# Optimization experiments

Hardware: AMD Instinct MI355X
Metric: run time of the kernel (lower is better)

The kernel has to match this reference:

```python
import jax, jax.numpy as jnp
import numpy as np

HEAD_DIM = 64
NUM_Q_HEADS = 32
NUM_KV_HEADS = 8
ROPE_FREQ = 10000.0
EPS = 1e-6


def _rms_norm(x, gamma):
    # normalize over last dim (head_dim)
    var = jnp.mean(jnp.square(x), axis=-1, keepdims=True)
    return x * jax.lax.rsqrt(var + EPS) * gamma


def _rope_cos_sin(seq_len, dtype=jnp.float32):
    inv_freq = 1.0 / (ROPE_FREQ ** (jnp.arange(0, HEAD_DIM, 2, dtype=jnp.float32) / HEAD_DIM))
    pos = jnp.arange(seq_len, dtype=jnp.float32)
    freqs = pos[:, None] * inv_freq[None, :]          # [S, hd/2]
    emb = jnp.concatenate([freqs, freqs], axis=-1)    # [S, hd]
    return jnp.cos(emb).astype(dtype), jnp.sin(emb).astype(dtype)


def _rotate_half(x):
    x1, x2 = jnp.split(x, 2, axis=-1)
    return jnp.concatenate([-x2, x1], axis=-1)


def _apply_rope(x, cos, sin):
    # x: [B, H, S, hd]; cos/sin: [S, hd]
    return x * cos[None, None, :, :] + _rotate_half(x) * sin[None, None, :, :]


def setup_inputs() -> dict:
    key = jax.random.key(0)
    ks = jax.random.split(key, 5)
    B, S, D = 2, 2048, 2048
    qkv_out = (NUM_Q_HEADS + 2 * NUM_KV_HEADS) * HEAD_DIM  # 3072
    x = jax.random.normal(ks[0], (B, S, D), dtype=jnp.float32)
    w_qkv = jax.random.normal(ks[1], (qkv_out, D), dtype=jnp.float32) * (D ** -0.5)
    w_out = jax.random.normal(ks[2], (D, NUM_Q_HEADS * HEAD_DIM), dtype=jnp.float32) * ((NUM_Q_HEADS * HEAD_DIM) ** -0.5)
    q_gamma = jnp.ones((HEAD_DIM,), dtype=jnp.float32)
    k_gamma = jnp.ones((HEAD_DIM,), dtype=jnp.float32)
    return {"x": x, "w_qkv": w_qkv, "w_out": w_out, "q_gamma": q_gamma, "k_gamma": k_gamma}


def reference(x, w_qkv, w_out, q_gamma, k_gamma):
    B, S, D = x.shape
    groups = NUM_Q_HEADS // NUM_KV_HEADS
    # fused QKV projection (no bias)
    qkv = jnp.einsum("bsd,od->bso", x, w_qkv)
    qkv = qkv.reshape(B, S, NUM_Q_HEADS + 2 * NUM_KV_HEADS, HEAD_DIM)
    qkv = jnp.transpose(qkv, (0, 2, 1, 3))  # [B, heads, S, hd]
    q = qkv[:, :NUM_Q_HEADS]
    k = qkv[:, NUM_Q_HEADS:NUM_Q_HEADS + NUM_KV_HEADS]
    v = qkv[:, NUM_Q_HEADS + NUM_KV_HEADS:]
    # QK RMSNorm over head_dim
    q = _rms_norm(q, q_gamma)
    k = _rms_norm(k, k_gamma)
    # RoPE
    cos, sin = _rope_cos_sin(S, dtype=x.dtype)
    q = _apply_rope(q, cos, sin)
    k = _apply_rope(k, cos, sin)
    # GQA: repeat-interleave kv heads
    k = jnp.repeat(k, groups, axis=1)
    v = jnp.repeat(v, groups, axis=1)
    # causal SDPA
    scale = HEAD_DIM ** -0.5
    scores = jnp.einsum("bhqd,bhkd->bhqk", q, k) * scale
    causal = jnp.tril(jnp.ones((S, S), dtype=bool))
    scores = jnp.where(causal[None, None], scores, jnp.finfo(scores.dtype).min)
    attn = jax.nn.softmax(scores, axis=-1)
    ctx = jnp.einsum("bhqk,bhkd->bhqd", attn, v)
    ctx = jnp.transpose(ctx, (0, 2, 1, 3)).reshape(B, S, NUM_Q_HEADS * HEAD_DIM)
    out = jnp.einsum("bsf,df->bsd", ctx, w_out)
    return out
```

## Files before the change

kernel.cpp:

```cpp
#include <hip/hip_runtime.h>

typedef _Float16 f16;
typedef __fp16 fp16x2 __attribute__((ext_vector_type(2)));
typedef _Float16 f16x8 __attribute__((ext_vector_type(8)));
typedef float f32x4 __attribute__((ext_vector_type(4)));
typedef float f32x16 __attribute__((ext_vector_type(16)));

#define AS1 __attribute__((address_space(1)))
#define AS3 __attribute__((address_space(3)))

#define SCALE_L2E 0.18033688011112042f


__device__ __forceinline__ void gload16(const void* g, void* l) {
    __builtin_amdgcn_global_load_lds(
        (const AS1 unsigned*)(unsigned long long)g,
        (AS3 unsigned*)(unsigned)(unsigned long long)l,
        16, 0, 0);
}

__device__ __forceinline__ unsigned pk2(float a, float b) {
    union { fp16x2 v; unsigned u; } c;
    c.v = __builtin_amdgcn_cvt_pkrtz(a, b);
    return c.u;
}

#define BAR() do { asm volatile("" ::: "memory"); __builtin_amdgcn_s_barrier(); asm volatile("" ::: "memory"); } while (0)


__global__ __launch_bounds__(256) void k_cast_all(const float* __restrict__ x,
                                                  const float* __restrict__ wq,
                                                  const float* __restrict__ wo,
                                                  f16* __restrict__ Xh,
                                                  f16* __restrict__ Wqh,
                                                  f16* __restrict__ Woh,
                                                  float* __restrict__ cosT,
                                                  float* __restrict__ sinT) {
    if (blockIdx.x >= 18432) {
        int idx = (blockIdx.x - 18432) * 256 + threadIdx.x;
        int s = idx >> 5, i = idx & 31;
        float ang = (float)s * exp2f(-(float)i * 0.4152410118609190f);
        cosT[idx] = cosf(ang);
        sinT[idx] = sinf(ang);
        return;
    }
    int i = (blockIdx.x * 256 + threadIdx.x) * 4;
    const float* src; f16* dst;
    if (i < 8388608)        { src = x  + i;            dst = Xh  + i; }
    else if (i < 14680064)  { src = wq + (i - 8388608); dst = Wqh + (i - 8388608); }
    else                    { src = wo + (i - 14680064); dst = Woh + (i - 14680064); }
    float4 v = *(const float4*)src;
    union { f16 h[4]; ushort4 u; } c;
    c.h[0] = (f16)v.x; c.h[1] = (f16)v.y; c.h[2] = (f16)v.z; c.h[3] = (f16)v.w;
    *(ushort4*)dst = c.u;
}


template <typename OutT, int BH>
__global__ __launch_bounds__(512, 2) void k_gemm256(const f16* __restrict__ A,
                                                    const f16* __restrict__ Bt,
                                                    OutT* __restrict__ C,
                                                    int M, int N, int K) {
    constexpr int BUFSZ = 32768 + BH * 16384;
    constexpr int NN = 2 * BH;
    __shared__ __align__(16) char sm[2 * BUFSZ];
    const int tid = threadIdx.x;
    const int lane = tid & 63, wid = tid >> 6;
    const int wm = wid >> 2, wn = wid & 3;
    const int lr = lane & 15, g4 = lane >> 4;

    const int gx = gridDim.x;
    const int nwg = gx * gridDim.y;
    int lin = blockIdx.y * gx + blockIdx.x;
    lin = (lin & 7) * (nwg >> 3) + (lin >> 3);
    const int bx = lin % gx, by = lin / gx;
    const int m0 = by * 256, n0 = bx * (128 * BH);
    const int NT = K >> 6;

    const int srow = tid >> 3;
    const int scol = ((tid & 7) ^ (srow & 7)) * 8;
    const f16* gA = A  + (size_t)(m0 + srow) * K + scol;
    const f16* gB = Bt + (size_t)(n0 + srow) * K + scol;

    auto STGA = [&](int t, int h) {
        char* d = sm + (t & 1) * BUFSZ + h * 16384 + tid * 16;
        gload16(gA + (size_t)(h * 128) * K + t * 64,      d);
        gload16(gA + (size_t)(h * 128 + 64) * K + t * 64, d + 8192);
    };
    auto STGB = [&](int t, int h) {
        char* d = sm + (t & 1) * BUFSZ + 32768 + h * 16384 + tid * 16;
        gload16(gB + (size_t)(h * 128) * K + t * 64,      d);
        gload16(gB + (size_t)(h * 128 + 64) * K + t * 64, d + 8192);
    };

    f32x4 acc[8][NN] = {};
    f16x8 bfr[NN];

    STGA(0, 0); STGA(0, 1); STGB(0, 0); if (BH == 2) STGB(0, 1);
    STGA(1, 0); STGA(1, 1); STGB(1, 0); if (BH == 2) STGB(1, 1);
    if constexpr (BH == 2) asm volatile("s_waitcnt vmcnt(8)" ::: "memory");
    else                   asm volatile("s_waitcnt vmcnt(6)" ::: "memory");
    BAR();

    for (int t = 0; t < NT; ++t) {
        const int buf = t & 1;
        const char* bA = sm + buf * BUFSZ + wm * 16384;
        const char* bB = sm + buf * BUFSZ + 32768 + (BH == 2 ? (wn >> 1) * 16384 : 0);
        const bool sA = (t >= 1) && (t + 1 < NT);
        const bool sB = (t + 2 < NT);
#pragma unroll
        for (int p = 0; p < 4; ++p) {
            const int kk = p >> 1, mh = p & 1;
            f16x8 afr[4];
            if (mh == 0) {
#pragma unroll
                for (int n = 0; n < NN; n++) {
                    const int r = (BH == 2 ? (wn & 1) * 64 : wn * 32) + n * 16 + lr;
                    bfr[n] = *(const f16x8*)(bB + ((r * 128 + kk * 64 + g4 * 16) ^ ((r & 7) << 4)));
                }
            }
#pragma unroll
            for (int i = 0; i < 4; i++) {
                const int r = (mh * 4 + i) * 16 + lr;
                afr[i] = *(const f16x8*)(bA + ((r * 128 + kk * 64 + g4 * 16) ^ ((r & 7) << 4)));
            }
            if (p == 0 && sA) STGA(t + 1, 0);
            if (p == 1 && sA) STGA(t + 1, 1);
            if (p == 3 && sB) { STGB(t + 2, 0); if (BH == 2) STGB(t + 2, 1); }
            BAR();
            asm volatile("s_waitcnt lgkmcnt(0)" ::: "memory");
            __builtin_amdgcn_s_setprio(1);
#pragma unroll
            for (int i = 0; i < 4; i++)
#pragma unroll
                for (int n = 0; n < NN; n++)
                    acc[mh * 4 + i][n] = __builtin_amdgcn_mfma_f32_16x16x32_f16(afr[i], bfr[n], acc[mh * 4 + i][n], 0, 0, 0);
            __builtin_amdgcn_s_setprio(0);
            if (p == 3 && t + 1 < NT) {
                if (t + 2 < NT) {
                    if constexpr (BH == 2) asm volatile("s_waitcnt vmcnt(4)" ::: "memory");
                    else                   asm volatile("s_waitcnt vmcnt(2)" ::: "memory");
                } else {
                    asm volatile("s_waitcnt vmcnt(0)" ::: "memory");
                }
            }
            BAR();
        }
    }

#pragma unroll
    for (int m = 0; m < 8; m++)
#pragma unroll
        for (int n = 0; n < NN; n++) {
            size_t base = (size_t)(m0 + wm * 128 + m * 16 + g4 * 4) * N + (n0 + wn * (32 * BH) + n * 16 + lr);
#pragma unroll
            for (int j = 0; j < 4; j++)
                C[base + (size_t)j * N] = (OutT)acc[m][n][j];
        }
}


__global__ __launch_bounds__(256) void k_qkv_post(const f16* __restrict__ qkv,
                                                  const float* __restrict__ qg,
                                                  const float* __restrict__ kg,
                                                  const float* __restrict__ cosT,
                                                  const float* __restrict__ sinT,
                                                  f16* __restrict__ Qf,
                                                  f16* __restrict__ Kf,
                                                  f16* __restrict__ Vf) {
    __shared__ f16 tl[4][8][72];
    const int tid = threadIdx.x, lane = tid & 63, wv = tid >> 6;
    const int gw = blockIdx.x * 4 + wv;
    const int b = gw / 12288;
    const int r0 = gw - b * 12288;
    const int head = r0 >> 8;
    const int sblk = r0 & 255;
    const int s0 = sblk * 8;
    const int s_loc = lane >> 3, ch = lane & 7;
    const int s = s0 + s_loc;

    f16x8 v = *(const f16x8*)&qkv[((size_t)b * 2048 + s) * 3072 + head * 64 + ch * 8];

    if (head < 40) {
        float vf[8];
#pragma unroll
        for (int j = 0; j < 8; j++) vf[j] = (float)v[j];
        float ss = 0.f;
#pragma unroll
        for (int j = 0; j < 8; j++) ss += vf[j] * vf[j];
        ss += __shfl_xor(ss, 1); ss += __shfl_xor(ss, 2); ss += __shfl_xor(ss, 4);
        float rinv = rsqrtf(ss * (1.0f / 64.0f) + 1e-6f);
        const float* gam = (head < 32 ? qg : kg) + ch * 8;
        float4 g0 = *(const float4*)gam, g1 = *(const float4*)(gam + 4);
        float gv[8] = {g0.x, g0.y, g0.z, g0.w, g1.x, g1.y, g1.z, g1.w};
        float xn[8], ot[8];
#pragma unroll
        for (int j = 0; j < 8; j++) xn[j] = vf[j] * rinv * gv[j];
#pragma unroll
        for (int j = 0; j < 8; j++) ot[j] = __shfl_xor(xn[j], 4);
        const int i0 = (ch & 3) * 8;
        float4 c0  = *(const float4*)&cosT[(s << 5) + i0];
        float4 c1  = *(const float4*)&cosT[(s << 5) + i0 + 4];
        float4 sn0 = *(const float4*)&sinT[(s << 5) + i0];
        float4 sn1 = *(const float4*)&sinT[(s << 5) + i0 + 4];
        float cs[8] = {c0.x, c0.y, c0.z, c0.w, c1.x, c1.y, c1.z, c1.w};
        float sn[8] = {sn0.x, sn0.y, sn0.z, sn0.w, sn1.x, sn1.y, sn1.z, sn1.w};
        float sgn = (ch < 4) ? -1.0f : 1.0f;
        float ov[8];
#pragma unroll
        for (int j = 0; j < 8; j++) ov[j] = xn[j] * cs[j] + sgn * ot[j] * sn[j];
        if (head < 32) {
#pragma unroll
            for (int j = 0; j < 8; j++) ov[j] *= SCALE_L2E;
        }
        uint4 o;
        o.x = pk2(ov[0], ov[1]); o.y = pk2(ov[2], ov[3]);
        o.z = pk2(ov[4], ov[5]); o.w = pk2(ov[6], ov[7]);
        const int t = s >> 5;
        const int lane2 = (s & 31) + ((ch & 1) << 5);
        const int c = ch >> 1;
        f16* dst = (head < 32)
            ? Qf + (((size_t)(b * 32 + head) * 256 + t * 4 + c) * 512 + lane2 * 8)
            : Kf + (((size_t)(b * 8 + head - 32) * 256 + t * 4 + c) * 512 + lane2 * 8);
        *(uint4*)dst = o;
    } else {
        const int kh = head - 40;
        *(f16x8*)&tl[wv][s_loc][ch * 8] = v;
        asm volatile("s_waitcnt lgkmcnt(0)" ::: "memory");
        f16x8 cv;
#pragma unroll
        for (int rr = 0; rr < 8; rr++) cv[rr] = tl[wv][rr][lane];
        const int d = lane, dh = d >> 5;
        const int t = s0 >> 5, c = (s0 >> 4) & 1, hv = (s0 >> 3) & 1;
        const int g = dh * 2 + c;
        f16* dst = Vf + (((size_t)(b * 8 + kh) * 256 + t * 4 + g) * 512
                         + ((d & 31) + (hv << 5)) * 8);
        *(f16x8*)dst = cv;
    }
}


struct AttnPart { f32x16 o0, o1; float l; };

__device__ __forceinline__ AttnPart attn_part(int qb, int par, int lane, int lq, int hi,
        const f16* __restrict__ Qfp, const f16* __restrict__ Kfp,
        const f16* __restrict__ Vfp) {
    f16x8 qf[4];
#pragma unroll
    for (int c = 0; c < 4; c++)
        qf[c] = *(const f16x8*)&Qfp[((size_t)qb * 4 + c) * 512 + lane * 8];

    AttnPart P;
    P.o0 = (f32x16){}; P.o1 = (f32x16){};
    float lrun = 0.0f;

    f16x8 kf[4], va[2], vb[2];
    if (par <= qb) {
#pragma unroll
        for (int c = 0; c < 4; c++)
            kf[c] = *(const f16x8*)&Kfp[((size_t)par * 4 + c) * 512 + lane * 8];
#pragma unroll
        for (int c = 0; c < 2; c++) {
            va[c] = *(const f16x8*)&Vfp[((size_t)par * 4 + c)     * 512 + lane * 8];
            vb[c] = *(const f16x8*)&Vfp[((size_t)par * 4 + 2 + c) * 512 + lane * 8];
        }
    }

    for (int kt = par; kt <= qb; kt += 2) {
        f32x16 st = {};
#pragma unroll
        for (int c = 0; c < 4; c++)
            st = __builtin_amdgcn_mfma_f32_32x32x16_f16(kf[c], qf[c], st, 0, 0, 0);

        if (kt + 2 <= qb) {
#pragma unroll
            for (int c = 0; c < 4; c++)
                kf[c] = *(const f16x8*)&Kfp[((size_t)(kt + 2) * 4 + c) * 512 + lane * 8];
        }

        if (kt == qb) {
#pragma unroll
            for (int r = 0; r < 16; r++) {
                int kvl = (r & 3) + ((r >> 2) << 3) + (hi << 2);
                if (kvl > lq) st[r] = -1e30f;
            }
        }

        unsigned X[8];
        float ps0 = 0.0f, ps1 = 0.0f;
#pragma unroll
        for (int j = 0; j < 8; j++) {
            float p0 = __builtin_amdgcn_exp2f(st[2 * j]);
            float p1 = __builtin_amdgcn_exp2f(st[2 * j + 1]);
            ps0 += p0; ps1 += p1;
            X[j] = pk2(p0, p1);
        }
        lrun += ps0 + ps1;

#pragma unroll
        for (int c = 0; c < 2; c++) {
            unsigned a0 = X[4 * c], a1 = X[4 * c + 1], a2 = X[4 * c + 2], a3 = X[4 * c + 3];
            asm volatile("v_permlane32_swap_b32 %0, %1" : "+v"(a0), "+v"(a2));
            asm volatile("v_permlane32_swap_b32 %0, %1" : "+v"(a1), "+v"(a3));
            union { unsigned u[4]; f16x8 v; } pb;
            pb.u[0] = a0; pb.u[1] = a1; pb.u[2] = a2; pb.u[3] = a3;
            P.o0 = __builtin_amdgcn_mfma_f32_32x32x16_f16(va[c], pb.v, P.o0, 0, 0, 0);
            P.o1 = __builtin_amdgcn_mfma_f32_32x32x16_f16(vb[c], pb.v, P.o1, 0, 0, 0);
        }
        if (kt + 2 <= qb) {
#pragma unroll
            for (int c = 0; c < 2; c++) {
                va[c] = *(const f16x8*)&Vfp[((size_t)(kt + 2) * 4 + c)     * 512 + lane * 8];
                vb[c] = *(const f16x8*)&Vfp[((size_t)(kt + 2) * 4 + 2 + c) * 512 + lane * 8];
            }
        }
    }

    P.l = lrun + __shfl_xor(lrun, 32);
    return P;
}

__global__ __launch_bounds__(128) void k_attn(const f16* __restrict__ Qf,
                                              const f16* __restrict__ Kf,
                                              const f16* __restrict__ Vf,
                                              f16* __restrict__ ctx) {
    __shared__ float ldsO[32][65];
    __shared__ float ldsL[32];
    const int tid = threadIdx.x;
    const int par = tid >> 6, lane = tid & 63;
    const int lq = lane & 31, hi = lane >> 5;
    const int bh = blockIdx.y, b = bh >> 5, h = bh & 31, kh = h >> 2;
    const int pj = blockIdx.x;

    const f16* Qfp = Qf + (size_t)(b * 32 + h) * 131072;
    const f16* Kfp = Kf + (size_t)(b * 8 + kh) * 131072;
    const f16* Vfp = Vf + (size_t)(b * 8 + kh) * 131072;
    f16*       ctxbase = ctx + (size_t)b * 2048 * 2048 + h * 64;

    const int qbs[2] = {pj, 63 - pj};
#pragma unroll
    for (int s = 0; s < 2; s++) {
        const int qb = qbs[s];
        AttnPart P = attn_part(qb, par, lane, lq, hi, Qfp, Kfp, Vfp);

        if (par == 1) {
            if (hi == 0) ldsL[lq] = P.l;
#pragma unroll
            for (int r = 0; r < 16; r++) {
                int d = (r & 3) + ((r >> 2) << 3) + (hi << 2);
                ldsO[lq][d]      = P.o0[r];
                ldsO[lq][d + 32] = P.o1[r];
            }
        }
        __syncthreads();
        if (par == 0) {
            float inv = 1.0f / (P.l + ldsL[lq]);
            unsigned* row = (unsigned*)(ctxbase + (size_t)(qb * 32 + lq) * 2048);
#pragma unroll
            for (int g = 0; g < 4; g++) {
                int d = 8 * g + 4 * hi;
                float c0 = (P.o0[4 * g]     + ldsO[lq][d])     * inv;
                float c1 = (P.o0[4 * g + 1] + ldsO[lq][d + 1]) * inv;
                float c2 = (P.o0[4 * g + 2] + ldsO[lq][d + 2]) * inv;
                float c3 = (P.o0[4 * g + 3] + ldsO[lq][d + 3]) * inv;
                uint2 a; a.x = pk2(c0, c1); a.y = pk2(c2, c3);
                *(uint2*)(row + 2 * hi + 4 * g) = a;
                float e0 = (P.o1[4 * g]     + ldsO[lq][d + 32]) * inv;
                float e1 = (P.o1[4 * g + 1] + ldsO[lq][d + 33]) * inv;
                float e2 = (P.o1[4 * g + 2] + ldsO[lq][d + 34]) * inv;
                float e3 = (P.o1[4 * g + 3] + ldsO[lq][d + 35]) * inv;
                uint2 e; e.x = pk2(e0, e1); e.y = pk2(e2, e3);
                *(uint2*)(row + 16 + 2 * hi + 4 * g) = e;
            }
        }
        __syncthreads();
    }
}


extern "C" void kernel_launch(void* const* d_in, const int* in_sizes, int n_in,
                              void* d_out, int out_size, void* d_ws, size_t ws_size,
                              hipStream_t stream) {
    const float* x     = (const float*)d_in[0];
    const float* w_qkv = (const float*)d_in[1];
    const float* w_out = (const float*)d_in[2];
    const float* qg    = (const float*)d_in[3];
    const float* kg    = (const float*)d_in[4];
    float* out = (float*)d_out;
    char* ws = (char*)d_ws;

    float* cosT = (float*)(ws);
    float* sinT = (float*)(ws + 262144);
    f16* Xh     = (f16*)(ws + 524288);
    f16* Wqkvh  = (f16*)(ws + 17301504);
    f16* Wouth  = (f16*)(ws + 29884416);
    f16* QKVh   = (f16*)(ws + 38273024);
    f16* Qfb    = (f16*)(ws + 63438848);
    f16* Kfb    = (f16*)(ws + 80216064);
    f16* Vfb    = (f16*)(ws + 84410368);
    f16* Ctxh   = (f16*)(ws + 88604672);

    k_cast_all<<<18688, 256, 0, stream>>>(x, w_qkv, w_out, Xh, Wqkvh, Wouth, cosT, sinT);

    k_gemm256<f16, 2><<<dim3(12, 16), 512, 0, stream>>>(Xh, Wqkvh, QKVh, 4096, 3072, 2048);

    k_qkv_post<<<6144, 256, 0, stream>>>(QKVh, qg, kg, cosT, sinT, Qfb, Kfb, Vfb);

    k_attn<<<dim3(32, 64), 128, 0, stream>>>(Qfb, Kfb, Vfb, Ctxh);

    k_gemm256<float, 1><<<dim3(16, 16), 512, 0, stream>>>(Ctxh, Wouth, out, 4096, 2048, 2048);
}
```

Measured before the change: 198.2 us.

## Generalize GEMM N-tile width and double-buffer K/V tiles in attention loop

The GEMM template now parameterizes its N tile in 64-column units. The QKV projection uses 192-wide tiles on a 16x16 grid, giving 256 workgroups instead of 192 so the CUs are filled more evenly. The output GEMM keeps its 128-wide tile through the new NU=2 path, with adjusted vmcnt waits. The attention inner loop is unrolled by two with separate register sets for K and V, so the score MFMA for the second tile overlaps the exp and PV of the first, at the cost of more registers.

```diff
diff --git a/kernel.cpp b/kernel.cpp
--- a/kernel.cpp
+++ b/kernel.cpp
@@ -56,13 +56,12 @@
 }
 
 
-template <typename OutT, int BH>
+template <typename OutT, int NU>
 __global__ __launch_bounds__(512, 2) void k_gemm256(const f16* __restrict__ A,
                                                     const f16* __restrict__ Bt,
                                                     OutT* __restrict__ C,
                                                     int M, int N, int K) {
-    constexpr int BUFSZ = 32768 + BH * 16384;
-    constexpr int NN = 2 * BH;
+    constexpr int BUFSZ = 32768 + NU * 8192;
     __shared__ __align__(16) char sm[2 * BUFSZ];
     const int tid = threadIdx.x;
     const int lane = tid & 63, wid = tid >> 6;
@@ -74,7 +73,7 @@
     int lin = blockIdx.y * gx + blockIdx.x;
     lin = (lin & 7) * (nwg >> 3) + (lin >> 3);
     const int bx = lin % gx, by = lin / gx;
-    const int m0 = by * 256, n0 = bx * (128 * BH);
+    const int m0 = by * 256, n0 = bx * (64 * NU);
     const int NT = K >> 6;
 
     const int srow = tid >> 3;
@@ -87,25 +86,26 @@
         gload16(gA + (size_t)(h * 128) * K + t * 64,      d);
         gload16(gA + (size_t)(h * 128 + 64) * K + t * 64, d + 8192);
     };
-    auto STGB = [&](int t, int h) {
-        char* d = sm + (t & 1) * BUFSZ + 32768 + h * 16384 + tid * 16;
-        gload16(gB + (size_t)(h * 128) * K + t * 64,      d);
-        gload16(gB + (size_t)(h * 128 + 64) * K + t * 64, d + 8192);
+    auto STGB = [&](int t) {
+#pragma unroll
+        for (int u = 0; u < NU; u++)
+            gload16(gB + (size_t)(u * 64) * K + t * 64,
+                    sm + (t & 1) * BUFSZ + 32768 + u * 8192 + tid * 16);
     };
 
-    f32x4 acc[8][NN] = {};
-    f16x8 bfr[NN];
-
-    STGA(0, 0); STGA(0, 1); STGB(0, 0); if (BH == 2) STGB(0, 1);
-    STGA(1, 0); STGA(1, 1); STGB(1, 0); if (BH == 2) STGB(1, 1);
-    if constexpr (BH == 2) asm volatile("s_waitcnt vmcnt(8)" ::: "memory");
-    else                   asm volatile("s_waitcnt vmcnt(6)" ::: "memory");
+    f32x4 acc[8][NU] = {};
+    f16x8 bfr[NU];
+
+    STGA(0, 0); STGA(0, 1); STGB(0);
+    STGA(1, 0); STGA(1, 1); STGB(1);
+    if constexpr (NU == 2) asm volatile("s_waitcnt vmcnt(6)" ::: "memory");
+    else                   asm volatile("s_waitcnt vmcnt(7)" ::: "memory");
     BAR();
 
     for (int t = 0; t < NT; ++t) {
         const int buf = t & 1;
         const char* bA = sm + buf * BUFSZ + wm * 16384;
-        const char* bB = sm + buf * BUFSZ + 32768 + (BH == 2 ? (wn >> 1) * 16384 : 0);
+        const char* bB = sm + buf * BUFSZ + 32768;
         const bool sA = (t >= 1) && (t + 1 < NT);
         const bool sB = (t + 2 < NT);
 #pragma unroll
@@ -114,8 +114,8 @@
             f16x8 afr[4];
             if (mh == 0) {
 #pragma unroll
-                for (int n = 0; n < NN; n++) {
-                    const int r = (BH == 2 ? (wn & 1) * 64 : wn * 32) + n * 16 + lr;
+                for (int n = 0; n < NU; n++) {
+                    const int r = wn * (16 * NU) + n * 16 + lr;
                     bfr[n] = *(const f16x8*)(bB + ((r * 128 + kk * 64 + g4 * 16) ^ ((r & 7) << 4)));
                 }
             }
@@ -126,20 +126,20 @@
             }
             if (p == 0 && sA) STGA(t + 1, 0);
             if (p == 1 && sA) STGA(t + 1, 1);
-            if (p == 3 && sB) { STGB(t + 2, 0); if (BH == 2) STGB(t + 2, 1); }
+            if (p == 3 && sB) STGB(t + 2);
             BAR();
             asm volatile("s_waitcnt lgkmcnt(0)" ::: "memory");
             __builtin_amdgcn_s_setprio(1);
 #pragma unroll
             for (int i = 0; i < 4; i++)
 #pragma unroll
-                for (int n = 0; n < NN; n++)
+                for (int n = 0; n < NU; n++)
                     acc[mh * 4 + i][n] = __builtin_amdgcn_mfma_f32_16x16x32_f16(afr[i], bfr[n], acc[mh * 4 + i][n], 0, 0, 0);
             __builtin_amdgcn_s_setprio(0);
             if (p == 3 && t + 1 < NT) {
                 if (t + 2 < NT) {
-                    if constexpr (BH == 2) asm volatile("s_waitcnt vmcnt(4)" ::: "memory");
-                    else                   asm volatile("s_waitcnt vmcnt(2)" ::: "memory");
+                    if constexpr (NU == 2) asm volatile("s_waitcnt vmcnt(2)" ::: "memory");
+                    else                   asm volatile("s_waitcnt vmcnt(3)" ::: "memory");
                 } else {
                     asm volatile("s_waitcnt vmcnt(0)" ::: "memory");
                 }
@@ -151,8 +151,8 @@
 #pragma unroll
     for (int m = 0; m < 8; m++)
 #pragma unroll
-        for (int n = 0; n < NN; n++) {
-            size_t base = (size_t)(m0 + wm * 128 + m * 16 + g4 * 4) * N + (n0 + wn * (32 * BH) + n * 16 + lr);
+        for (int n = 0; n < NU; n++) {
+            size_t base = (size_t)(m0 + wm * 128 + m * 16 + g4 * 4) * N + (n0 + wn * (16 * NU) + n * 16 + lr);
 #pragma unroll
             for (int j = 0; j < 4; j++)
                 C[base + (size_t)j * N] = (OutT)acc[m][n][j];
@@ -242,6 +242,40 @@
 
 struct AttnPart { f32x16 o0, o1; float l; };
 
+__device__ __forceinline__ void do_exp(const f32x16& st, unsigned* X, float& lrun) {
+    float ps0 = 0.0f, ps1 = 0.0f;
+#pragma unroll
+    for (int j = 0; j < 8; j++) {
+        float p0 = __builtin_amdgcn_exp2f(st[2 * j]);
+        float p1 = __builtin_amdgcn_exp2f(st[2 * j + 1]);
+        ps0 += p0; ps1 += p1;
+        X[j] = pk2(p0, p1);
+    }
+    lrun += ps0 + ps1;
+}
+
+__device__ __forceinline__ void do_pv(const f16x8* va, const f16x8* vb,
+                                      const unsigned* X, f32x16& o0, f32x16& o1) {
+#pragma unroll
+    for (int c = 0; c < 2; c++) {
+        unsigned a0 = X[4 * c], a1 = X[4 * c + 1], a2 = X[4 * c + 2], a3 = X[4 * c + 3];
+        asm volatile("v_permlane32_swap_b32 %0, %1" : "+v"(a0), "+v"(a2));
+        asm volatile("v_permlane32_swap_b32 %0, %1" : "+v"(a1), "+v"(a3));
+        union { unsigned u[4]; f16x8 v; } pb;
+        pb.u[0] = a0; pb.u[1] = a1; pb.u[2] = a2; pb.u[3] = a3;
+        o0 = __builtin_amdgcn_mfma_f32_32x32x16_f16(va[c], pb.v, o0, 0, 0, 0);
+        o1 = __builtin_amdgcn_mfma_f32_32x32x16_f16(vb[c], pb.v, o1, 0, 0, 0);
+    }
+}
+
+__device__ __forceinline__ void do_mask(f32x16& st, int lq, int hi) {
+#pragma unroll
+    for (int r = 0; r < 16; r++) {
+        int kvl = (r & 3) + ((r >> 2) << 3) + (hi << 2);
+        if (kvl > lq) st[r] = -1e30f;
+    }
+}
+
 __device__ __forceinline__ AttnPart attn_part(int qb, int par, int lane, int lq, int hi,
         const f16* __restrict__ Qfp, const f16* __restrict__ Kfp,
         const f16* __restrict__ Vfp) {
@@ -254,66 +288,62 @@
     P.o0 = (f32x16){}; P.o1 = (f32x16){};
     float lrun = 0.0f;
 
-    f16x8 kf[4], va[2], vb[2];
-    if (par <= qb) {
+    f16x8 kfa[4], kfb[4], vaa[2], vba[2], vab[2], vbb[2];
+
+    auto LOADK = [&](f16x8* kf, int t) {
 #pragma unroll
         for (int c = 0; c < 4; c++)
-            kf[c] = *(const f16x8*)&Kfp[((size_t)par * 4 + c) * 512 + lane * 8];
+            kf[c] = *(const f16x8*)&Kfp[((size_t)t * 4 + c) * 512 + lane * 8];
+    };
+    auto LOADV = [&](f16x8* va, f16x8* vb, int t) {
 #pragma unroll
         for (int c = 0; c < 2; c++) {
-            va[c] = *(const f16x8*)&Vfp[((size_t)par * 4 + c)     * 512 + lane * 8];
-            vb[c] = *(const f16x8*)&Vfp[((size_t)par * 4 + 2 + c) * 512 + lane * 8];
-        }
-    }
-
-    for (int kt = par; kt <= qb; kt += 2) {
+            va[c] = *(const f16x8*)&Vfp[((size_t)t * 4 + c)     * 512 + lane * 8];
+            vb[c] = *(const f16x8*)&Vfp[((size_t)t * 4 + 2 + c) * 512 + lane * 8];
+        }
+    };
+
+    int kt = par;
+    if (kt <= qb)     { LOADK(kfa, kt);     LOADV(vaa, vba, kt); }
+    if (kt + 2 <= qb) { LOADK(kfb, kt + 2); LOADV(vab, vbb, kt + 2); }
+
+    while (kt + 2 <= qb) {
+        const int nx = kt + 4;
+        f32x16 sta = {};
+#pragma unroll
+        for (int c = 0; c < 4; c++)
+            sta = __builtin_amdgcn_mfma_f32_32x32x16_f16(kfa[c], qf[c], sta, 0, 0, 0);
+        unsigned Xa[8];
+        do_exp(sta, Xa, lrun);
+
+        f32x16 stb = {};
+#pragma unroll
+        for (int c = 0; c < 4; c++)
+            stb = __builtin_amdgcn_mfma_f32_32x32x16_f16(kfb[c], qf[c], stb, 0, 0, 0);
+        if (nx <= qb) LOADK(kfa, nx);
+
+        do_pv(vaa, vba, Xa, P.o0, P.o1);
+        if (nx <= qb) LOADV(vaa, vba, nx);
+
+        if (kt + 2 == qb) do_mask(stb, lq, hi);
+        unsigned Xb[8];
+        do_exp(stb, Xb, lrun);
+        if (nx + 2 <= qb) LOADK(kfb, nx + 2);
+
+        do_pv(vab, vbb, Xb, P.o0, P.o1);
+        if (nx + 2 <= qb) LOADV(vab, vbb, nx + 2);
+
+        kt = nx;
+    }
+    if (kt <= qb) {
         f32x16 st = {};
 #pragma unroll
         for (int c = 0; c < 4; c++)
-            st = __builtin_amdgcn_mfma_f32_32x32x16_f16(kf[c], qf[c], st, 0, 0, 0);
-
-        if (kt + 2 <= qb) {
-#pragma unroll
-            for (int c = 0; c < 4; c++)
-                kf[c] = *(const f16x8*)&Kfp[((size_t)(kt + 2) * 4 + c) * 512 + lane * 8];
-        }
-
-        if (kt == qb) {
-#pragma unroll
-            for (int r = 0; r < 16; r++) {
-                int kvl = (r & 3) + ((r >> 2) << 3) + (hi << 2);
-                if (kvl > lq) st[r] = -1e30f;
-            }
-        }
-
+            st = __builtin_amdgcn_mfma_f32_32x32x16_f16(kfa[c], qf[c], st, 0, 0, 0);
+        if (kt == qb) do_mask(st, lq, hi);
         unsigned X[8];
-        float ps0 = 0.0f, ps1 = 0.0f;
-#pragma unroll
-        for (int j = 0; j < 8; j++) {
-            float p0 = __builtin_amdgcn_exp2f(st[2 * j]);
-            float p1 = __builtin_amdgcn_exp2f(st[2 * j + 1]);
-            ps0 += p0; ps1 += p1;
-            X[j] = pk2(p0, p1);
-        }
-        lrun += ps0 + ps1;
-
-#pragma unroll
-        for (int c = 0; c < 2; c++) {
-            unsigned a0 = X[4 * c], a1 = X[4 * c + 1], a2 = X[4 * c + 2], a3 = X[4 * c + 3];
-            asm volatile("v_permlane32_swap_b32 %0, %1" : "+v"(a0), "+v"(a2));
-            asm volatile("v_permlane32_swap_b32 %0, %1" : "+v"(a1), "+v"(a3));
-            union { unsigned u[4]; f16x8 v; } pb;
-            pb.u[0] = a0; pb.u[1] = a1; pb.u[2] = a2; pb.u[3] = a3;
-            P.o0 = __builtin_amdgcn_mfma_f32_32x32x16_f16(va[c], pb.v, P.o0, 0, 0, 0);
-            P.o1 = __builtin_amdgcn_mfma_f32_32x32x16_f16(vb[c], pb.v, P.o1, 0, 0, 0);
-        }
-        if (kt + 2 <= qb) {
-#pragma unroll
-            for (int c = 0; c < 2; c++) {
-                va[c] = *(const f16x8*)&Vfp[((size_t)(kt + 2) * 4 + c)     * 512 + lane * 8];
-                vb[c] = *(const f16x8*)&Vfp[((size_t)(kt + 2) * 4 + 2 + c) * 512 + lane * 8];
-            }
-        }
+        do_exp(st, X, lrun);
+        do_pv(vaa, vba, X, P.o0, P.o1);
     }
 
     P.l = lrun + __shfl_xor(lrun, 32);
@@ -402,11 +432,11 @@
 
     k_cast_all<<<18688, 256, 0, stream>>>(x, w_qkv, w_out, Xh, Wqkvh, Wouth, cosT, sinT);
 
-    k_gemm256<f16, 2><<<dim3(12, 16), 512, 0, stream>>>(Xh, Wqkvh, QKVh, 4096, 3072, 2048);
+    k_gemm256<f16, 3><<<dim3(16, 16), 512, 0, stream>>>(Xh, Wqkvh, QKVh, 4096, 3072, 2048);
 
     k_qkv_post<<<6144, 256, 0, stream>>>(QKVh, qg, kg, cosT, sinT, Qfb, Kfb, Vfb);
 
     k_attn<<<dim3(32, 64), 128, 0, stream>>>(Qfb, Kfb, Vfb, Ctxh);
 
-    k_gemm256<float, 1><<<dim3(16, 16), 512, 0, stream>>>(Ctxh, Wouth, out, 4096, 2048, 2048);
-}
+    k_gemm256<float, 2><<<dim3(16, 16), 512, 0, stream>>>(Ctxh, Wouth, out, 4096, 2048, 2048);
+}
```

New measurement: 187.1 us (median of 2 runs). -5.6%, faster.
